# Optimization experiments

Measured on AMD Instinct MI355X. Metric: run time of the kernel, lower is better.

Reference implementation:

```python
import jax, jax.numpy as jnp
import numpy as np

N, E, D, H = 100000, 1600000, 128, 128


def setup_inputs() -> dict:
    key = jax.random.key(0)
    ks = jax.random.split(key, 7)
    x = jax.random.normal(ks[0], (N, D), dtype=jnp.float32)
    edge_index = jax.random.randint(ks[1], (2, E), 0, N, dtype=jnp.int64)
    edge_weight = jax.random.uniform(ks[2], (E,), dtype=jnp.float32)
    s = 1.0 / np.sqrt(D)
    W0 = jax.random.normal(ks[3], (D, H), dtype=jnp.float32) * s
    b0 = jnp.zeros((H,), dtype=jnp.float32)
    W1 = jax.random.normal(ks[4], (H, H), dtype=jnp.float32) * (1.0 / np.sqrt(H))
    b1 = jnp.zeros((H,), dtype=jnp.float32)
    return {"x": x, "edge_weight": edge_weight, "W0": W0, "b0": b0,
            "W1": W1, "b1": b1, "edge_index": edge_index}


def reference(x, edge_weight, W0, b0, W1, b1, edge_index):
    src, dst = edge_index[0], edge_index[1]
    n = x.shape[0]
    # gcn_norm with self-loops (fill_value=1): deg includes the self-loop weight
    deg = jax.ops.segment_sum(edge_weight, dst, num_segments=n) + 1.0  # [N]
    dis = jnp.where(deg > 0, jax.lax.rsqrt(deg), 0.0)                  # deg^-1/2
    norm = dis[src] * edge_weight * dis[dst]                           # [E]
    self_coef = dis * dis                                              # self-loop norm = 1/deg

    def gcn_layer(h, W, b):
        hW = h @ W                                                     # [N,H]
        agg = jax.ops.segment_sum(norm[:, None] * hW[src], dst, num_segments=n)
        agg = agg + self_coef[:, None] * hW                            # self-loop term
        return jax.nn.relu(agg + b)

    h1 = gcn_layer(x, W0, b0)
    h2 = gcn_layer(h1, W1, b1)
    return jnp.concatenate([h1, h2], axis=1)  # [N, 2H]
```

## Files before the change

kernel.cpp:

```cpp
#include <hip/hip_runtime.h>
#include <hip/hip_fp16.h>


typedef unsigned int u32;
typedef _Float16 f16;
typedef f16 f16x4 __attribute__((ext_vector_type(4)));
typedef f16 f16x8 __attribute__((ext_vector_type(8)));
typedef float f32x4 __attribute__((ext_vector_type(4)));

__global__ __launch_bounds__(256) void k_wfrag(const float* __restrict__ W0,
                                               const float* __restrict__ W1,
                                               __half* __restrict__ Wf) {
    int idx = blockIdx.x * 256 + threadIdx.x;
    const float* W = (idx < 2048) ? W0 : W1;
    int id = idx & 2047;
    int l = id & 63, nt = (id >> 6) & 7, ks = id >> 9;
    int nn = nt * 16 + (l & 15);
    int kb = ks * 32 + ((l >> 4) & 3) * 4;
    union { int4 v; __half h[8]; } pk;
#pragma unroll
    for (int j = 0; j < 8; ++j) {
        int k = kb + (j & 3) + 16 * (j >> 2);
        pk.h[j] = __float2half(W[k * 128 + nn]);
    }
    *(int4*)(Wf + (size_t)idx * 8) = pk.v;
}

__device__ __forceinline__ void gemm_body(const float* __restrict__ A, int lda,
                                          const __half* __restrict__ Wf,
                                          __half* __restrict__ C, int n,
                                          int bid, int t) {
    const int w2 = t >> 6, l = t & 63;
    const int node = bid * 64 + w2 * 16 + (l & 15);
    const int koff = ((l >> 4) & 3) * 4;
    const bool ok = node < n;
    const float* ap = A + (size_t)(ok ? node : 0) * lda;

    f16x8 af[4];
#pragma unroll
    for (int ks = 0; ks < 4; ++ks) {
        float4 a0 = make_float4(0.f, 0.f, 0.f, 0.f), a1 = a0;
        if (ok) {
            a0 = *(const float4*)(ap + ks * 32 + koff);
            a1 = *(const float4*)(ap + ks * 32 + koff + 16);
        }
        f16x8 h;
        h[0] = (f16)a0.x; h[1] = (f16)a0.y; h[2] = (f16)a0.z; h[3] = (f16)a0.w;
        h[4] = (f16)a1.x; h[5] = (f16)a1.y; h[6] = (f16)a1.z; h[7] = (f16)a1.w;
        af[ks] = h;
    }

    f32x4 acc[8];
#pragma unroll
    for (int i = 0; i < 8; ++i) acc[i] = (f32x4){0.f, 0.f, 0.f, 0.f};

#pragma unroll
    for (int ks = 0; ks < 4; ++ks) {
#pragma unroll
        for (int nt = 0; nt < 8; ++nt) {
            f16x8 wf = *(const f16x8*)(Wf + ((size_t)(ks * 8 + nt) * 64 + l) * 8);
            acc[nt] = __builtin_amdgcn_mfma_f32_16x16x32_f16(wf, af[ks], acc[nt], 0, 0, 0);
        }
    }

    if (ok) {
        const int c0 = ((l >> 4) & 3) * 4;
#pragma unroll
        for (int nt = 0; nt < 8; ++nt) {
            union { short4 s4; __half h[4]; } pk;
#pragma unroll
            for (int r2 = 0; r2 < 4; ++r2) pk.h[r2] = __float2half(acc[nt][r2]);
            *(short4*)(C + (size_t)node * 128 + nt * 16 + c0) = pk.s4;
        }
    }
}

__global__ __launch_bounds__(256) void k_p1gemm(const int* __restrict__ dst,
                                                u32* __restrict__ H,
                                                int e, int NB, int nch,
                                                const float* __restrict__ A, int lda,
                                                const __half* __restrict__ Wf,
                                                __half* __restrict__ C, int n) {
    const int bid = blockIdx.x, t = threadIdx.x;
    if (bid >= nch) {
        gemm_body(A, lda, Wf, C, n, bid - nch, t);
        return;
    }
    __shared__ u32 lcnt[512];
    lcnt[t] = 0; lcnt[t + 256] = 0;
    __syncthreads();
    int i0 = bid * 4096 + t;
#pragma unroll
    for (int u = 0; u < 16; ++u) {
        int i = i0 + u * 256;
        if (i < e) atomicAdd(&lcnt[(u32)dst[i] >> 9], 1u);
    }
    __syncthreads();
    for (int b = t; b < NB; b += 256) H[(size_t)b * nch + bid] = lcnt[b];
}

__global__ __launch_bounds__(256) void k_scan1(u32* data, u32* sums, int n) {
    __shared__ u32 tmp[256];
    int gid = blockIdx.x * 256 + threadIdx.x;
    u32 v = (gid < n) ? data[gid] : 0;
    tmp[threadIdx.x] = v;
    __syncthreads();
    for (int off = 1; off < 256; off <<= 1) {
        u32 t = (threadIdx.x >= off) ? tmp[threadIdx.x - off] : 0;
        __syncthreads();
        tmp[threadIdx.x] += t;
        __syncthreads();
    }
    if (gid < n) data[gid] = tmp[threadIdx.x] - v;
    if (threadIdx.x == 255) sums[blockIdx.x] = tmp[255];
}

__global__ __launch_bounds__(512) void k_scan2(u32* sums, int nb) {
    __shared__ u32 tmp[512];
    u32 v = (threadIdx.x < nb) ? sums[threadIdx.x] : 0;
    tmp[threadIdx.x] = v;
    __syncthreads();
    for (int off = 1; off < 512; off <<= 1) {
        u32 t = (threadIdx.x >= off) ? tmp[threadIdx.x - off] : 0;
        __syncthreads();
        tmp[threadIdx.x] += t;
        __syncthreads();
    }
    if (threadIdx.x < nb) sums[threadIdx.x] = tmp[threadIdx.x] - v;
}

__global__ __launch_bounds__(256) void k_p2(const int* __restrict__ src,
                                            const int* __restrict__ dst,
                                            const float* __restrict__ w,
                                            const u32* __restrict__ H,
                                            const u32* __restrict__ S,
                                            int2* __restrict__ tmp,
                                            int e, int NB, int nch) {
    __shared__ u32 lcnt[512];
    __shared__ u32 lbase[512];
    const int t = threadIdx.x, bid = blockIdx.x;
    lcnt[t] = 0; lcnt[t + 256] = 0;
    __syncthreads();
    for (int b = t; b < NB; b += 256) {
        u32 idx = (u32)b * nch + bid;
        lbase[b] = H[idx] + S[idx >> 8];
    }
    __syncthreads();
    int i0 = bid * 4096 + t;
#pragma unroll
    for (int u = 0; u < 16; ++u) {
        int i = i0 + u * 256;
        if (i < e) {
            int d = dst[i];
            u32 b = (u32)d >> 9;
            u32 lr = atomicAdd(&lcnt[b], 1u);
            tmp[lbase[b] + lr] = make_int2(src[i] | ((d & 511) << 17),
                                           __float_as_int(w[i]));
        }
    }
}

__global__ __launch_bounds__(512) void k_p3a(const int2* __restrict__ tmp,
                                             const u32* __restrict__ H,
                                             const u32* __restrict__ S,
                                             int* __restrict__ rowstart,
                                             float* __restrict__ dis,
                                             int e, int n, int NB, int nch) {
    const int bid = blockIdx.x, t = threadIdx.x;
    __shared__ u32 cnt[512];
    __shared__ u32 degx[512];
    __shared__ u32 stmp[512];

    cnt[t] = 0; degx[t] = 0;
    __syncthreads();

    u32 i0 = (u32)bid * nch;
    const int bs = (int)(H[i0] + S[i0 >> 8]);
    u32 i1 = (u32)(bid + 1) * nch;
    const int be = (bid + 1 < NB) ? (int)(H[i1] + S[i1 >> 8]) : e;

    for (int j = bs + t; j < be; j += 512) {
        int2 r = tmp[j];
        u32 low = ((u32)r.x >> 17) & 511u;
        atomicAdd(&cnt[low], 1u);
        atomicAdd(&degx[low], (u32)(__int_as_float(r.y) * 1048576.0f + 0.5f));
    }
    __syncthreads();

    u32 v = cnt[t];
    stmp[t] = v;
    __syncthreads();
    for (int o = 1; o < 512; o <<= 1) {
        u32 x = (t >= o) ? stmp[t - o] : 0u;
        __syncthreads();
        stmp[t] += x;
        __syncthreads();
    }

    const int node = bid * 512 + t;
    if (node < n) {
        rowstart[node] = bs + (int)(stmp[t] - v);
        dis[node] = rsqrtf(1.0f + (float)degx[t] * (1.0f / 1048576.0f));
    }
}

__global__ __launch_bounds__(512) void k_p3b(const int2* __restrict__ tmp,
                                             const u32* __restrict__ H,
                                             const u32* __restrict__ S,
                                             const int* __restrict__ rowstart,
                                             const float* __restrict__ dis,
                                             int2* __restrict__ ep,
                                             int e, int n, int NB, int nch) {
    const int bid = blockIdx.x, t = threadIdx.x;
    __shared__ u32 cur[512];
    const int node = bid * 512 + t;
    cur[t] = (node < n) ? (u32)rowstart[node] : 0u;
    __syncthreads();

    u32 i0 = (u32)bid * nch;
    const int bs = (int)(H[i0] + S[i0 >> 8]);
    u32 i1 = (u32)(bid + 1) * nch;
    const int be = (bid + 1 < NB) ? (int)(H[i1] + S[i1 >> 8]) : e;

    for (int j = bs + t; j < be; j += 512) {
        int2 r = tmp[j];
        u32 low = ((u32)r.x >> 17) & 511u;
        int s = r.x & 0x1FFFF;
        float wd = __int_as_float(r.y) * dis[s];
        u32 p = atomicAdd(&cur[low], 1u);
        ep[p] = make_int2(s, __float_as_int(wd));
    }
}

__device__ __forceinline__ float2 agg_row(const __half* __restrict__ hW, int ldh,
                                          const int2* __restrict__ ep,
                                          int start, int end, int lane,
                                          float2 acc) {
    int j = start;
    for (; j + 15 < end; j += 16) {
        int2 r[16];
        __half2 v[16];
#pragma unroll
        for (int u = 0; u < 16; ++u) r[u] = ep[j + u];
#pragma unroll
        for (int u = 0; u < 16; ++u)
            v[u] = *(const __half2*)(hW + (size_t)r[u].x * ldh + lane * 2);
#pragma unroll
        for (int u = 0; u < 16; ++u) {
            float nm = __int_as_float(r[u].y);
            float2 f = __half22float2(v[u]);
            acc.x += nm * f.x;
            acc.y += nm * f.y;
        }
    }
    for (; j + 7 < end; j += 8) {
        int2 r[8];
        __half2 v[8];
#pragma unroll
        for (int u = 0; u < 8; ++u) r[u] = ep[j + u];
#pragma unroll
        for (int u = 0; u < 8; ++u)
            v[u] = *(const __half2*)(hW + (size_t)r[u].x * ldh + lane * 2);
#pragma unroll
        for (int u = 0; u < 8; ++u) {
            float nm = __int_as_float(r[u].y);
            float2 f = __half22float2(v[u]);
            acc.x += nm * f.x;
            acc.y += nm * f.y;
        }
    }
    for (; j + 3 < end; j += 4) {
        int2 r[4];
        __half2 v[4];
#pragma unroll
        for (int u = 0; u < 4; ++u) r[u] = ep[j + u];
#pragma unroll
        for (int u = 0; u < 4; ++u)
            v[u] = *(const __half2*)(hW + (size_t)r[u].x * ldh + lane * 2);
#pragma unroll
        for (int u = 0; u < 4; ++u) {
            float nm = __int_as_float(r[u].y);
            float2 f = __half22float2(v[u]);
            acc.x += nm * f.x;
            acc.y += nm * f.y;
        }
    }
    for (; j < end; ++j) {
        int2 rec = ep[j];
        float nm = __int_as_float(rec.y);
        float2 v = __half22float2(*(const __half2*)(hW + (size_t)rec.x * ldh + lane * 2));
        acc.x += nm * v.x;
        acc.y += nm * v.y;
    }
    return acc;
}

__global__ __launch_bounds__(256) void k_aggemm(const __half* __restrict__ hW1,
                                                const int2* __restrict__ ep,
                                                const int* __restrict__ rowstart,
                                                const float* __restrict__ dis,
                                                const float* __restrict__ bias,
                                                float* __restrict__ outcol,
                                                const __half* __restrict__ Wf2,
                                                __half* __restrict__ hW2,
                                                int n, int e) {
    __shared__ f16 As[16][132];
    const int t = threadIdx.x;
    const int w2 = t >> 6, lane = t & 63;

    float2 b = *(const float2*)(bias + lane * 2);

#pragma unroll
    for (int i = 0; i < 4; ++i) {
        const int lr = w2 * 4 + i;
        const int wid = blockIdx.x * 16 + lr;
        if (wid < n) {
            int start = rowstart[wid];
            int end   = (wid == n - 1) ? e : rowstart[wid + 1];
            start = __builtin_amdgcn_readfirstlane(start);
            end   = __builtin_amdgcn_readfirstlane(end);

            const float dd = dis[wid];
            float2 h = __half22float2(*(const __half2*)(hW1 + (size_t)wid * 128 + lane * 2));
            float2 acc;
            acc.x = dd * h.x;
            acc.y = dd * h.y;
            acc = agg_row(hW1, 128, ep, start, end, lane, acc);

            float ox = fmaxf(dd * acc.x + b.x, 0.f);
            float oy = fmaxf(dd * acc.y + b.y, 0.f);
            *(float2*)(outcol + (size_t)wid * 256 + lane * 2) = make_float2(ox, oy);
            As[lr][2 * lane]     = (f16)ox;
            As[lr][2 * lane + 1] = (f16)oy;
        } else {
            As[lr][2 * lane]     = (f16)0.f;
            As[lr][2 * lane + 1] = (f16)0.f;
        }
    }
    __syncthreads();

    const int koff = ((lane >> 4) & 3) * 4;
    f32x4 acc2[2];
    acc2[0] = (f32x4){0.f, 0.f, 0.f, 0.f};
    acc2[1] = (f32x4){0.f, 0.f, 0.f, 0.f};

#pragma unroll
    for (int ks = 0; ks < 4; ++ks) {
        f16x4 lo = *(const f16x4*)&As[lane & 15][ks * 32 + koff];
        f16x4 hi = *(const f16x4*)&As[lane & 15][ks * 32 + koff + 16];
        f16x8 af;
        af[0] = lo[0]; af[1] = lo[1]; af[2] = lo[2]; af[3] = lo[3];
        af[4] = hi[0]; af[5] = hi[1]; af[6] = hi[2]; af[7] = hi[3];
#pragma unroll
        for (int q = 0; q < 2; ++q) {
            const int nt = w2 * 2 + q;
            f16x8 wf = *(const f16x8*)(Wf2 + ((size_t)(ks * 8 + nt) * 64 + lane) * 8);
            acc2[q] = __builtin_amdgcn_mfma_f32_16x16x32_f16(wf, af, acc2[q], 0, 0, 0);
        }
    }

    const int node = blockIdx.x * 16 + (lane & 15);
    if (node < n) {
        const int c0 = ((lane >> 4) & 3) * 4;
#pragma unroll
        for (int q = 0; q < 2; ++q) {
            const int nt = w2 * 2 + q;
            union { short4 s4; __half h[4]; } pk;
#pragma unroll
            for (int r2 = 0; r2 < 4; ++r2) pk.h[r2] = __float2half(acc2[q][r2]);
            *(short4*)(hW2 + (size_t)node * 128 + nt * 16 + c0) = pk.s4;
        }
    }
}

__global__ __launch_bounds__(256) void k_agg(const __half* __restrict__ hW,
                                             const int2* __restrict__ ep,
                                             const int* __restrict__ rowstart,
                                             const float* __restrict__ dis,
                                             const float* __restrict__ bias,
                                             float* __restrict__ outcol,
                                             int n, int e) {
    int wid = blockIdx.x * 4 + (threadIdx.x >> 6);
    int lane = threadIdx.x & 63;
    if (wid >= n) return;

    int start = rowstart[wid];
    int end   = (wid == n - 1) ? e : rowstart[wid + 1];
    start = __builtin_amdgcn_readfirstlane(start);
    end   = __builtin_amdgcn_readfirstlane(end);

    const float dd = dis[wid];
    float2 h = __half22float2(*(const __half2*)(hW + (size_t)wid * 128 + lane * 2));
    float2 acc;
    acc.x = dd * h.x;
    acc.y = dd * h.y;
    acc = agg_row(hW, 128, ep, start, end, lane, acc);

    float2 b = *(const float2*)(bias + lane * 2);
    float2 o;
    o.x = fmaxf(dd * acc.x + b.x, 0.f);
    o.y = fmaxf(dd * acc.y + b.y, 0.f);
    *(float2*)(outcol + (size_t)wid * 256 + lane * 2) = o;
}

extern "C" void kernel_launch(void* const* d_in, const int* in_sizes, int n_in,
                              void* d_out, int out_size, void* d_ws, size_t ws_size,
                              hipStream_t stream) {
    const float* x  = (const float*)d_in[0];
    const float* ew = (const float*)d_in[1];
    const float* W0 = (const float*)d_in[2];
    const float* b0 = (const float*)d_in[3];
    const float* W1 = (const float*)d_in[4];
    const float* b1 = (const float*)d_in[5];
    const int*   ei = (const int*)d_in[6];

    const int N = in_sizes[0] / 128;
    const int E = in_sizes[1];
    const int* src = ei;
    const int* dst = ei + E;
    float* out = (float*)d_out;

    const int NB  = (N + 511) >> 9;
    const int nch = (E + 4095) >> 12;
    const int scanN = NB * nch;
    const int scanB = (scanN + 255) / 256;
    const int gT = (N + 63) / 64;
    const int gF = (N + 15) / 16;
    const int gA = (N + 3) / 4;

    const size_t Hsz  = (size_t)((scanN + 1) & ~1);
    const size_t Npad = (size_t)((N + 1) & ~1);
    u32*   H        = (u32*)d_ws;
    u32*   sums     = H + Hsz;
    int*   rowstart = (int*)(sums + 512);
    float* dis      = (float*)(rowstart + Npad);
    int2*  ep       = (int2*)(dis + Npad);
    __half* hW1     = (__half*)(ep + E);
    __half* Wf      = hW1 + (size_t)N * 128;
    int2*  tmp      = (int2*)(Wf + 32768);
    __half* hW2     = (__half*)tmp;

    k_wfrag<<<16, 256, 0, stream>>>(W0, W1, Wf);
    k_p1gemm<<<nch + gT, 256, 0, stream>>>(dst, H, E, NB, nch, x, 128, Wf, hW1, N);
    k_scan1<<<scanB, 256, 0, stream>>>(H, sums, scanN);
    k_scan2<<<1, 512, 0, stream>>>(sums, scanB);
    k_p2<<<nch, 256, 0, stream>>>(src, dst, ew, H, sums, tmp, E, NB, nch);
    k_p3a<<<NB, 512, 0, stream>>>(tmp, H, sums, rowstart, dis, E, N, NB, nch);
    k_p3b<<<NB, 512, 0, stream>>>(tmp, H, sums, rowstart, dis, ep, E, N, NB, nch);

    k_aggemm<<<gF, 256, 0, stream>>>(hW1, ep, rowstart, dis, b0, out,
                                     Wf + 16384, hW2, N, E);

    k_agg<<<gA, 256, 0, stream>>>(hW2, ep, rowstart, dis, b1, out + 128, N, E);
}
```

Measured before the change: 260.0 us.

## Split layer-1 GEMM across CSR-build kernels and fuse weight packing into histogram

The x@W0 GEMM moves out of the histogram kernel and is split into two halves. Those halves run as extra blocks inside the p3a and p3b CSR-build kernels, and the weight-fragment packing moves into the histogram kernel as extra blocks. This fills the under-occupied p3a/p3b launches with independent work and removes a separate k_wfrag launch. Output stores in both aggregation kernels become nontemporal to avoid polluting cache. The cost is added tile-indexing complexity and the risk of imbalance between the mixed block types.

After: 286.8 us. 1.1x slower.

```diff
diff --git a/kernel.cpp b/kernel.cpp
--- a/kernel.cpp
+++ b/kernel.cpp
@@ -8,22 +8,10 @@
 typedef f16 f16x8 __attribute__((ext_vector_type(8)));
 typedef float f32x4 __attribute__((ext_vector_type(4)));
 
-__global__ __launch_bounds__(256) void k_wfrag(const float* __restrict__ W0,
-                                               const float* __restrict__ W1,
-                                               __half* __restrict__ Wf) {
-    int idx = blockIdx.x * 256 + threadIdx.x;
-    const float* W = (idx < 2048) ? W0 : W1;
-    int id = idx & 2047;
-    int l = id & 63, nt = (id >> 6) & 7, ks = id >> 9;
-    int nn = nt * 16 + (l & 15);
-    int kb = ks * 32 + ((l >> 4) & 3) * 4;
-    union { int4 v; __half h[8]; } pk;
-#pragma unroll
-    for (int j = 0; j < 8; ++j) {
-        int k = kb + (j & 3) + 16 * (j >> 2);
-        pk.h[j] = __float2half(W[k * 128 + nn]);
-    }
-    *(int4*)(Wf + (size_t)idx * 8) = pk.v;
+__device__ __forceinline__ void st_nt_f2(float* p, float ox, float oy) {
+    union { double d; float f[2]; } u;
+    u.f[0] = ox; u.f[1] = oy;
+    __builtin_nontemporal_store(u.d, (double*)p);
 }
 
 __device__ __forceinline__ void gemm_body(const float* __restrict__ A, int lda,
@@ -75,15 +63,27 @@
     }
 }
 
-__global__ __launch_bounds__(256) void k_p1gemm(const int* __restrict__ dst,
-                                                u32* __restrict__ H,
-                                                int e, int NB, int nch,
-                                                const float* __restrict__ A, int lda,
-                                                const __half* __restrict__ Wf,
-                                                __half* __restrict__ C, int n) {
+__global__ __launch_bounds__(256) void k_p1(const int* __restrict__ dst,
+                                            u32* __restrict__ H,
+                                            int e, int NB, int nch,
+                                            const float* __restrict__ W0,
+                                            const float* __restrict__ W1,
+                                            __half* __restrict__ Wf) {
     const int bid = blockIdx.x, t = threadIdx.x;
     if (bid >= nch) {
-        gemm_body(A, lda, Wf, C, n, bid - nch, t);
+        int idx = (bid - nch) * 256 + t;
+        const float* W = (idx < 2048) ? W0 : W1;
+        int id = idx & 2047;
+        int l = id & 63, nt = (id >> 6) & 7, ks = id >> 9;
+        int nn = nt * 16 + (l & 15);
+        int kb = ks * 32 + ((l >> 4) & 3) * 4;
+        union { int4 v; __half h[8]; } pk;
+#pragma unroll
+        for (int j = 0; j < 8; ++j) {
+            int k = kb + (j & 3) + 16 * (j >> 2);
+            pk.h[j] = __float2half(W[k * 128 + nn]);
+        }
+        *(int4*)(Wf + (size_t)idx * 8) = pk.v;
         return;
     }
     __shared__ u32 lcnt[512];
@@ -165,8 +165,16 @@
                                              const u32* __restrict__ S,
                                              int* __restrict__ rowstart,
                                              float* __restrict__ dis,
-                                             int e, int n, int NB, int nch) {
+                                             int e, int n, int NB, int nch,
+                                             const float* __restrict__ A, int lda,
+                                             const __half* __restrict__ Wf,
+                                             __half* __restrict__ C, int tileOff) {
     const int bid = blockIdx.x, t = threadIdx.x;
+    if (bid >= NB) {
+        int g = (bid - NB) * 2 + (t >> 8) + tileOff;
+        gemm_body(A, lda, Wf, C, n, g, t & 255);
+        return;
+    }
     __shared__ u32 cnt[512];
     __shared__ u32 degx[512];
     __shared__ u32 stmp[512];
@@ -210,8 +218,16 @@
                                              const int* __restrict__ rowstart,
                                              const float* __restrict__ dis,
                                              int2* __restrict__ ep,
-                                             int e, int n, int NB, int nch) {
+                                             int e, int n, int NB, int nch,
+                                             const float* __restrict__ A, int lda,
+                                             const __half* __restrict__ Wf,
+                                             __half* __restrict__ C, int tileOff) {
     const int bid = blockIdx.x, t = threadIdx.x;
+    if (bid >= NB) {
+        int g = (bid - NB) * 2 + (t >> 8) + tileOff;
+        gemm_body(A, lda, Wf, C, n, g, t & 255);
+        return;
+    }
     __shared__ u32 cur[512];
     const int node = bid * 512 + t;
     cur[t] = (node < n) ? (u32)rowstart[node] : 0u;
@@ -329,7 +345,7 @@
 
             float ox = fmaxf(dd * acc.x + b.x, 0.f);
             float oy = fmaxf(dd * acc.y + b.y, 0.f);
-            *(float2*)(outcol + (size_t)wid * 256 + lane * 2) = make_float2(ox, oy);
+            st_nt_f2(outcol + (size_t)wid * 256 + lane * 2, ox, oy);
             As[lr][2 * lane]     = (f16)ox;
             As[lr][2 * lane + 1] = (f16)oy;
         } else {
@@ -397,10 +413,9 @@
     acc = agg_row(hW, 128, ep, start, end, lane, acc);
 
     float2 b = *(const float2*)(bias + lane * 2);
-    float2 o;
-    o.x = fmaxf(dd * acc.x + b.x, 0.f);
-    o.y = fmaxf(dd * acc.y + b.y, 0.f);
-    *(float2*)(outcol + (size_t)wid * 256 + lane * 2) = o;
+    float ox = fmaxf(dd * acc.x + b.x, 0.f);
+    float oy = fmaxf(dd * acc.y + b.y, 0.f);
+    st_nt_f2(outcol + (size_t)wid * 256 + lane * 2, ox, oy);
 }
 
 extern "C" void kernel_launch(void* const* d_in, const int* in_sizes, int n_in,
@@ -425,6 +440,10 @@
     const int scanN = NB * nch;
     const int scanB = (scanN + 255) / 256;
     const int gT = (N + 63) / 64;
+    const int tilesA = ((gT + 1) / 2 + 1) & ~1;
+    const int blocksA = tilesA / 2;
+    const int tilesB = gT - tilesA;
+    const int blocksB = (tilesB + 1) / 2;
     const int gF = (N + 15) / 16;
     const int gA = (N + 3) / 4;
 
@@ -440,13 +459,14 @@
     int2*  tmp      = (int2*)(Wf + 32768);
     __half* hW2     = (__half*)tmp;
 
-    k_wfrag<<<16, 256, 0, stream>>>(W0, W1, Wf);
-    k_p1gemm<<<nch + gT, 256, 0, stream>>>(dst, H, E, NB, nch, x, 128, Wf, hW1, N);
+    k_p1<<<nch + 16, 256, 0, stream>>>(dst, H, E, NB, nch, W0, W1, Wf);
     k_scan1<<<scanB, 256, 0, stream>>>(H, sums, scanN);
     k_scan2<<<1, 512, 0, stream>>>(sums, scanB);
     k_p2<<<nch, 256, 0, stream>>>(src, dst, ew, H, sums, tmp, E, NB, nch);
-    k_p3a<<<NB, 512, 0, stream>>>(tmp, H, sums, rowstart, dis, E, N, NB, nch);
-    k_p3b<<<NB, 512, 0, stream>>>(tmp, H, sums, rowstart, dis, ep, E, N, NB, nch);
+    k_p3a<<<NB + blocksA, 512, 0, stream>>>(tmp, H, sums, rowstart, dis, E, N, NB, nch,
+                                            x, 128, Wf, hW1, 0);
+    k_p3b<<<NB + blocksB, 512, 0, stream>>>(tmp, H, sums, rowstart, dis, ep, E, N, NB, nch,
+                                            x, 128, Wf, hW1, tilesA);
 
     k_aggemm<<<gF, 256, 0, stream>>>(hW1, ep, rowstart, dis, b0, out,
                                      Wf + 16384, hW2, N, E);
```
